# Optimization experiments

Measured on AMD Instinct MI355X. Metric: run time of the kernel, lower is better.

The kernel has to match this reference:

```python
import jax, jax.numpy as jnp
import numpy as np

EPS = 1e-8
LN_EPS = 1e-5

def _layernorm(x, g, b):
    mu = jnp.mean(x, axis=-1, keepdims=True)
    var = jnp.mean((x - mu) ** 2, axis=-1, keepdims=True)
    return (x - mu) / jnp.sqrt(var + LN_EPS) * g + b

def setup_inputs() -> dict:
    key = jax.random.key(0)
    ks = jax.random.split(key, 10)
    B, S = 8192, 4096
    input_dim, hidden_dim = 4, 256
    h4 = hidden_dim // 4  # 64
    price_series = jax.random.uniform(ks[0], (B, S, 1), dtype=jnp.float32) + 0.5
    # 4 parallel encoders stacked on leading axis: Linear(input_dim->h4) + LayerNorm(h4)
    enc_w = jax.random.normal(ks[1], (4, input_dim, h4), dtype=jnp.float32) * 0.5
    enc_b = jax.random.normal(ks[2], (4, h4), dtype=jnp.float32) * 0.02
    enc_g = jnp.ones((4, h4), dtype=jnp.float32)
    enc_beta = jnp.zeros((4, h4), dtype=jnp.float32)
    # regime head: Linear(hidden_dim->64) + ReLU + (Dropout eval=identity) + Linear(64->4)
    head_w1 = jax.random.normal(ks[3], (hidden_dim, 64), dtype=jnp.float32) * 0.0625
    head_b1 = jnp.zeros((64,), dtype=jnp.float32)
    head_w2 = jax.random.normal(ks[4], (64, 4), dtype=jnp.float32) * 0.125
    head_b2 = jnp.zeros((4,), dtype=jnp.float32)
    return {"price_series": price_series, "enc_w": enc_w, "enc_b": enc_b,
            "enc_g": enc_g, "enc_beta": enc_beta,
            "head_w1": head_w1, "head_b1": head_b1,
            "head_w2": head_w2, "head_b2": head_b2}

def reference(price_series, enc_w, enc_b, enc_g, enc_beta, head_w1, head_b1, head_w2, head_b2):
    prices = price_series[:, :, 0]  # [B, S]
    B, S = prices.shape
    # Rolling SMA(20) with clamped window start, via cumsum (single pass, no per-step loop)
    csum = jnp.concatenate([jnp.zeros((B, 1), prices.dtype), jnp.cumsum(prices, axis=1)], axis=1)  # [B, S+1]
    i = jnp.arange(S)
    start20 = jnp.maximum(0, i - 19)
    cnt20 = (i - start20 + 1).astype(prices.dtype)
    sma20 = (csum[:, i + 1] - csum[:, start20]) / cnt20  # [B, S]
    trend_signal = (prices - sma20) / (sma20 + EPS)
    f_trend = jnp.mean(trend_signal, axis=1, keepdims=True)  # [B,1]
    # momentum over last 10 steps
    p_last = prices[:, -1:]
    p_m10 = prices[:, -10:-9]
    f_mom = (p_last - p_m10) / (p_m10 + EPS)  # [B,1]
    # mean reversion
    p_mean = jnp.mean(prices, axis=1, keepdims=True)
    f_mr = (p_last - p_mean) / (p_mean + EPS)  # [B,1]
    # cycle: coefficient of variation (torch.std is unbiased, ddof=1)
    f_cyc = jnp.std(prices, axis=1, ddof=1, keepdims=True) / (p_mean + EPS)  # [B,1]
    combined = jnp.concatenate([f_trend, f_mom, f_mr, f_cyc], axis=1)  # [B, 4]
    # 4 parallel encoders: Linear -> ReLU -> LayerNorm
    pre = jnp.einsum('bi,eio->ebo', combined, enc_w) + enc_b[:, None, :]  # [4, B, 64]
    feats = _layernorm(jax.nn.relu(pre), enc_g[:, None, :], enc_beta[:, None, :])  # [4, B, 64]
    # concat order: trend, momentum, mean_rev, cycle along feature dim
    regime_features = jnp.transpose(feats, (1, 0, 2)).reshape(B, -1)  # [B, 256]
    h = jax.nn.relu(regime_features @ head_w1 + head_b1)
    regime_probs = jax.nn.softmax(h @ head_w2 + head_b2, axis=1)  # [B, 4]
    return (regime_features, regime_probs)
```

## Files before the change

### kernel.cpp

```cpp
#include <hip/hip_runtime.h>

#define EPS 1e-8f
#define LN_EPS 1e-5f
#define NROWS 8192
#define SLEN 4096
#define PROBS_OFF 2097152

typedef __attribute__((ext_vector_type(8))) short bf16x8;
typedef __attribute__((ext_vector_type(4))) float f32x4;

__device__ __forceinline__ short f2bf(float f) {
    unsigned u = __float_as_uint(f);
    unsigned r = (u + 0x7FFFu + ((u >> 16) & 1u)) >> 16;
    return (short)r;
}

#define SLP(i) ((i) + ((((i) >> 4)) << 2))

__global__ __launch_bounds__(256) void k_feat(const float* __restrict__ prices,
                                              float* __restrict__ comb) {
    __shared__ float sld[SLEN + (SLEN >> 2)];
    __shared__ float red[12];

    const int t = threadIdx.x;
    const int b = blockIdx.x;
    const int lane = t & 63, wv = t >> 6;
    const float4* rowp4 = (const float4*)(prices + (size_t)b * SLEN);

    #pragma unroll
    for (int i = 0; i < 4; ++i) {
        int m = i * 256 + t;
        float4 v = rowp4[m];
        *(float4*)&sld[SLP(4 * m)] = v;
    }
    __syncthreads();

    const int p0 = t * 16;
    float4 s0 = *(const float4*)&sld[SLP(p0)];
    float4 s1 = *(const float4*)&sld[SLP(p0 + 4)];
    float4 s2 = *(const float4*)&sld[SLP(p0 + 8)];
    float4 s3 = *(const float4*)&sld[SLP(p0 + 12)];
    float4 q0, q1, q2, q3, q4;
    if (t > 0) {
        q0 = *(const float4*)&sld[SLP(p0 - 20)];
        q1 = *(const float4*)&sld[SLP(p0 - 16)];
        q2 = *(const float4*)&sld[SLP(p0 - 12)];
        q3 = *(const float4*)&sld[SLP(p0 - 8)];
        q4 = *(const float4*)&sld[SLP(p0 - 4)];
    } else {
        q0 = q1 = q2 = q3 = q4 = make_float4(0.f, 0.f, 0.f, 0.f);
    }

    float xv[16] = { s0.x, s0.y, s0.z, s0.w, s1.x, s1.y, s1.z, s1.w,
                     s2.x, s2.y, s2.z, s2.w, s3.x, s3.y, s3.z, s3.w };
    float ov[16] = { q0.x, q0.y, q0.z, q0.w, q1.x, q1.y, q1.z, q1.w,
                     q2.x, q2.y, q2.z, q2.w, q3.x, q3.y, q3.z, q3.w };

    float W = q0.y + q0.z + q0.w
            + q1.x + q1.y + q1.z + q1.w
            + q2.x + q2.y + q2.z + q2.w
            + q3.x + q3.y + q3.z + q3.w
            + q4.x + q4.y + q4.z + q4.w;

    float sum = 0.0f, sq = 0.0f, ts = 0.0f;
    #pragma unroll
    for (int j = 0; j < 16; ++j) {
        float x = xv[j];
        W += (j == 0) ? x : (x - ov[j]);
        sum += x;
        sq = fmaf(x, x, sq);
        float c = fminf((float)(p0 + j + 1), 20.0f);
        float sm = W * __builtin_amdgcn_rcpf(c);
        ts += (x - sm) * __builtin_amdgcn_rcpf(sm + EPS);
    }

    #pragma unroll
    for (int off = 32; off > 0; off >>= 1) {
        sum += __shfl_xor(sum, off);
        sq  += __shfl_xor(sq,  off);
        ts  += __shfl_xor(ts,  off);
    }
    if (lane == 0) { red[wv * 3] = sum; red[wv * 3 + 1] = sq; red[wv * 3 + 2] = ts; }
    __syncthreads();

    if (t == 0) {
        float S = red[0] + red[3] + red[6] + red[9];
        float Q = red[1] + red[4] + red[7] + red[10];
        float T = red[2] + red[5] + red[8] + red[11];
        float mean = S * (1.0f / 4096.0f);
        float var  = fmaxf((Q - 4096.0f * mean * mean) * (1.0f / 4095.0f), 0.0f);
        float p_last = sld[SLP(4095)];
        float p_m10  = sld[SLP(4086)];
        float4 c;
        c.x = T * (1.0f / 4096.0f);
        c.y = (p_last - p_m10) / (p_m10 + EPS);
        c.z = (p_last - mean) / (mean + EPS);
        c.w = sqrtf(var) / (mean + EPS);
        *(float4*)(comb + (size_t)b * 4) = c;
    }
}

#define ROWS 32

__global__ __launch_bounds__(256) void k_head(
    const float* __restrict__ combg, float* __restrict__ out,
    const float* __restrict__ enc_w, const float* __restrict__ enc_b,
    const float* __restrict__ enc_g, const float* __restrict__ enc_bt,
    const float* __restrict__ w1, const float* __restrict__ b1,
    const float* __restrict__ w2, const float* __restrict__ b2)
{
    __shared__ float comb[ROWS][4];
    __shared__ short rfb[ROWS][264];
    __shared__ float hbuf[ROWS][68];

    const int t = threadIdx.x;
    const int r0 = blockIdx.x * ROWS;
    const int lane = t & 63, wave = t >> 6;
    const int l15 = lane & 15, q = lane >> 4;

    if (t < ROWS * 4)
        comb[t >> 2][t & 3] = combg[(size_t)(r0 + (t >> 2)) * 4 + (t & 3)];

    bf16x8 bfrag[8];
    #pragma unroll
    for (int kt = 0; kt < 8; ++kt) {
        #pragma unroll
        for (int j = 0; j < 8; ++j) {
            int k = kt * 32 + q * 8 + j;
            bfrag[kt][j] = f2bf(w1[k * 64 + wave * 16 + l15]);
        }
    }

    const float ew0 = enc_w[wave * 256 + lane];
    const float ew1v = enc_w[wave * 256 + 64 + lane];
    const float ew2v = enc_w[wave * 256 + 128 + lane];
    const float ew3v = enc_w[wave * 256 + 192 + lane];
    const float ebv = enc_b[t], egv = enc_g[t], btv = enc_bt[t];

    __syncthreads();

    for (int r = 0; r < ROWS; ++r) {
        float4 cb = *(const float4*)comb[r];
        float v = fmaf(cb.x, ew0, fmaf(cb.y, ew1v, fmaf(cb.z, ew2v, fmaf(cb.w, ew3v, ebv))));
        v = fmaxf(v, 0.0f);
        float sm = v;
        #pragma unroll
        for (int off = 32; off > 0; off >>= 1) sm += __shfl_xor(sm, off);
        float mu = sm * (1.0f / 64.0f);
        float d = v - mu;
        float vs = d * d;
        #pragma unroll
        for (int off = 32; off > 0; off >>= 1) vs += __shfl_xor(vs, off);
        float y = fmaf(d * rsqrtf(vs * (1.0f / 64.0f) + LN_EPS), egv, btv);
        out[(size_t)(r0 + r) * 256 + t] = y;
        rfb[r][t] = f2bf(y);
    }
    __syncthreads();

    f32x4 acc0 = {0.f, 0.f, 0.f, 0.f}, acc1 = {0.f, 0.f, 0.f, 0.f};
    #pragma unroll
    for (int kt = 0; kt < 8; ++kt) {
        bf16x8 a0 = *(const bf16x8*)&rfb[l15][kt * 32 + q * 8];
        bf16x8 a1 = *(const bf16x8*)&rfb[16 + l15][kt * 32 + q * 8];
        acc0 = __builtin_amdgcn_mfma_f32_16x16x32_bf16(a0, bfrag[kt], acc0, 0, 0, 0);
        acc1 = __builtin_amdgcn_mfma_f32_16x16x32_bf16(a1, bfrag[kt], acc1, 0, 0, 0);
    }

    const int col = wave * 16 + l15;
    const float b1v = b1[col];
    #pragma unroll
    for (int rg = 0; rg < 4; ++rg) {
        hbuf[q * 4 + rg][col]      = fmaxf(acc0[rg] + b1v, 0.0f);
        hbuf[16 + q * 4 + rg][col] = fmaxf(acc1[rg] + b1v, 0.0f);
    }
    __syncthreads();

    if (t < 128) {
        int r = t >> 2, c = t & 3;
        float lg = b2[c];
        #pragma unroll
        for (int j = 0; j < 64; ++j) lg = fmaf(hbuf[r][j], w2[j * 4 + c], lg);
        float mx = fmaxf(lg, __shfl_xor(lg, 1, 4));
        mx = fmaxf(mx, __shfl_xor(mx, 2, 4));
        float ex = __expf(lg - mx);
        float s2 = ex + __shfl_xor(ex, 1, 4);
        s2 += __shfl_xor(s2, 2, 4);
        out[PROBS_OFF + (size_t)(r0 + r) * 4 + c] = ex / s2;
    }
}

extern "C" void kernel_launch(void* const* d_in, const int* in_sizes, int n_in,
                              void* d_out, int out_size, void* d_ws, size_t ws_size,
                              hipStream_t stream) {
    const float* prices  = (const float*)d_in[0];
    const float* enc_w   = (const float*)d_in[1];
    const float* enc_b   = (const float*)d_in[2];
    const float* enc_g   = (const float*)d_in[3];
    const float* enc_bt  = (const float*)d_in[4];
    const float* head_w1 = (const float*)d_in[5];
    const float* head_b1 = (const float*)d_in[6];
    const float* head_w2 = (const float*)d_in[7];
    const float* head_b2 = (const float*)d_in[8];
    float* out  = (float*)d_out;
    float* comb = (float*)d_ws;

    k_feat<<<NROWS, 256, 0, stream>>>(prices, comb);
    k_head<<<NROWS / ROWS, 256, 0, stream>>>(comb, out, enc_w, enc_b, enc_g, enc_bt,
                                             head_w1, head_b1, head_w2, head_b2);
}
```

Baseline: 221.4 us.

## Split each price row across two blocks and finalize features in head kernel

The feature kernel now launches two blocks per row, each handling half the sequence with an 8-element-per-thread loop and a 20-element halo loaded into a smaller shared buffer. Each half writes partial sums (sum, sum of squares, trend sum) to workspace, plus the last prices. The head kernel combines the halves and computes the four features. This doubles the block count and shrinks per-block LDS to raise occupancy and latency hiding for the memory-bound scan. In exchange it re-reads halo data and adds a little extra workspace traffic.

Measured after the change: 221.1 us. No clear change (-0.1%).

```diff
diff --git a/kernel.cpp b/kernel.cpp
--- a/kernel.cpp
+++ b/kernel.cpp
@@ -18,43 +18,40 @@
 #define SLP(i) ((i) + ((((i) >> 4)) << 2))
 
 __global__ __launch_bounds__(256) void k_feat(const float* __restrict__ prices,
-                                              float* __restrict__ comb) {
-    __shared__ float sld[SLEN + (SLEN >> 2)];
+                                              float* __restrict__ ws) {
+    __shared__ float sld[2596];
     __shared__ float red[12];
 
     const int t = threadIdx.x;
-    const int b = blockIdx.x;
+    const int b = blockIdx.x >> 1, h = blockIdx.x & 1;
     const int lane = t & 63, wv = t >> 6;
     const float4* rowp4 = (const float4*)(prices + (size_t)b * SLEN);
 
-    #pragma unroll
-    for (int i = 0; i < 4; ++i) {
-        int m = i * 256 + t;
-        float4 v = rowp4[m];
-        *(float4*)&sld[SLP(4 * m)] = v;
-    }
-    __syncthreads();
-
-    const int p0 = t * 16;
-    float4 s0 = *(const float4*)&sld[SLP(p0)];
-    float4 s1 = *(const float4*)&sld[SLP(p0 + 4)];
-    float4 s2 = *(const float4*)&sld[SLP(p0 + 8)];
-    float4 s3 = *(const float4*)&sld[SLP(p0 + 12)];
-    float4 q0, q1, q2, q3, q4;
-    if (t > 0) {
-        q0 = *(const float4*)&sld[SLP(p0 - 20)];
-        q1 = *(const float4*)&sld[SLP(p0 - 16)];
-        q2 = *(const float4*)&sld[SLP(p0 - 12)];
-        q3 = *(const float4*)&sld[SLP(p0 - 8)];
-        q4 = *(const float4*)&sld[SLP(p0 - 4)];
-    } else {
-        q0 = q1 = q2 = q3 = q4 = make_float4(0.f, 0.f, 0.f, 0.f);
-    }
-
-    float xv[16] = { s0.x, s0.y, s0.z, s0.w, s1.x, s1.y, s1.z, s1.w,
-                     s2.x, s2.y, s2.z, s2.w, s3.x, s3.y, s3.z, s3.w };
-    float ov[16] = { q0.x, q0.y, q0.z, q0.w, q1.x, q1.y, q1.z, q1.w,
-                     q2.x, q2.y, q2.z, q2.w, q3.x, q3.y, q3.z, q3.w };
+    {
+        int f0 = t, f1 = t + 256;
+        int g0 = 512 * h - 8 + f0, g1 = 512 * h - 8 + f1;
+        float4 v0 = (g0 >= 0) ? rowp4[g0] : make_float4(0.f, 0.f, 0.f, 0.f);
+        float4 v1 = rowp4[g1];
+        *(float4*)&sld[SLP(4 * f0)] = v0;
+        *(float4*)&sld[SLP(4 * f1)] = v1;
+        if (t < 8) {
+            int f2 = 512 + t;
+            *(float4*)&sld[SLP(4 * f2)] = rowp4[512 * h - 8 + f2];
+        }
+    }
+    __syncthreads();
+
+    const int li0 = 32 + 8 * t;
+    float4 s0 = *(const float4*)&sld[SLP(li0)];
+    float4 s1 = *(const float4*)&sld[SLP(li0 + 4)];
+    float4 q0 = *(const float4*)&sld[SLP(li0 - 20)];
+    float4 q1 = *(const float4*)&sld[SLP(li0 - 16)];
+    float4 q2 = *(const float4*)&sld[SLP(li0 - 12)];
+    float4 q3 = *(const float4*)&sld[SLP(li0 - 8)];
+    float4 q4 = *(const float4*)&sld[SLP(li0 - 4)];
+
+    float xv[8] = { s0.x, s0.y, s0.z, s0.w, s1.x, s1.y, s1.z, s1.w };
+    float ov[8] = { q0.x, q0.y, q0.z, q0.w, q1.x, q1.y, q1.z, q1.w };
 
     float W = q0.y + q0.z + q0.w
             + q1.x + q1.y + q1.z + q1.w
@@ -62,17 +59,21 @@
             + q3.x + q3.y + q3.z + q3.w
             + q4.x + q4.y + q4.z + q4.w;
 
+    const float pf = (float)(2048 * h + 8 * t);
     float sum = 0.0f, sq = 0.0f, ts = 0.0f;
     #pragma unroll
-    for (int j = 0; j < 16; ++j) {
+    for (int j = 0; j < 8; ++j) {
         float x = xv[j];
         W += (j == 0) ? x : (x - ov[j]);
         sum += x;
         sq = fmaf(x, x, sq);
-        float c = fminf((float)(p0 + j + 1), 20.0f);
+        float c = fminf(pf + (float)(j + 1), 20.0f);
         float sm = W * __builtin_amdgcn_rcpf(c);
         ts += (x - sm) * __builtin_amdgcn_rcpf(sm + EPS);
     }
+
+    if (h == 1 && t == 254) ws[(size_t)b * 8 + 6] = xv[6];
+    if (h == 1 && t == 255) ws[(size_t)b * 8 + 7] = xv[7];
 
     #pragma unroll
     for (int off = 32; off > 0; off >>= 1) {
@@ -87,23 +88,15 @@
         float S = red[0] + red[3] + red[6] + red[9];
         float Q = red[1] + red[4] + red[7] + red[10];
         float T = red[2] + red[5] + red[8] + red[11];
-        float mean = S * (1.0f / 4096.0f);
-        float var  = fmaxf((Q - 4096.0f * mean * mean) * (1.0f / 4095.0f), 0.0f);
-        float p_last = sld[SLP(4095)];
-        float p_m10  = sld[SLP(4086)];
-        float4 c;
-        c.x = T * (1.0f / 4096.0f);
-        c.y = (p_last - p_m10) / (p_m10 + EPS);
-        c.z = (p_last - mean) / (mean + EPS);
-        c.w = sqrtf(var) / (mean + EPS);
-        *(float4*)(comb + (size_t)b * 4) = c;
+        float* wp = ws + (size_t)b * 8 + 3 * h;
+        wp[0] = S; wp[1] = Q; wp[2] = T;
     }
 }
 
 #define ROWS 32
 
 __global__ __launch_bounds__(256) void k_head(
-    const float* __restrict__ combg, float* __restrict__ out,
+    const float* __restrict__ ws, float* __restrict__ out,
     const float* __restrict__ enc_w, const float* __restrict__ enc_b,
     const float* __restrict__ enc_g, const float* __restrict__ enc_bt,
     const float* __restrict__ w1, const float* __restrict__ b1,
@@ -118,8 +111,19 @@
     const int lane = t & 63, wave = t >> 6;
     const int l15 = lane & 15, q = lane >> 4;
 
-    if (t < ROWS * 4)
-        comb[t >> 2][t & 3] = combg[(size_t)(r0 + (t >> 2)) * 4 + (t & 3)];
+    if (t < ROWS) {
+        const float* wp = ws + (size_t)(r0 + t) * 8;
+        float4 a = *(const float4*)wp;
+        float4 bb = *(const float4*)(wp + 4);
+        float S = a.x + a.w, Q = a.y + bb.x, T = a.z + bb.y;
+        float p_m10 = bb.z, p_last = bb.w;
+        float mean = S * (1.0f / 4096.0f);
+        float var  = fmaxf((Q - 4096.0f * mean * mean) * (1.0f / 4095.0f), 0.0f);
+        comb[t][0] = T * (1.0f / 4096.0f);
+        comb[t][1] = (p_last - p_m10) / (p_m10 + EPS);
+        comb[t][2] = (p_last - mean) / (mean + EPS);
+        comb[t][3] = sqrtf(var) / (mean + EPS);
+    }
 
     bf16x8 bfrag[8];
     #pragma unroll
@@ -201,10 +205,10 @@
     const float* head_b1 = (const float*)d_in[6];
     const float* head_w2 = (const float*)d_in[7];
     const float* head_b2 = (const float*)d_in[8];
-    float* out  = (float*)d_out;
-    float* comb = (float*)d_ws;
-
-    k_feat<<<NROWS, 256, 0, stream>>>(prices, comb);
-    k_head<<<NROWS / ROWS, 256, 0, stream>>>(comb, out, enc_w, enc_b, enc_g, enc_bt,
+    float* out = (float*)d_out;
+    float* ws  = (float*)d_ws;
+
+    k_feat<<<NROWS * 2, 256, 0, stream>>>(prices, ws);
+    k_head<<<NROWS / ROWS, 256, 0, stream>>>(ws, out, enc_w, enc_b, enc_g, enc_bt,
                                              head_w1, head_b1, head_w2, head_b2);
 }
```
